# Optimization experiments

Measured on AMD Instinct MI355X. Metric: run time of the kernel, lower is better.

The kernel has to match this reference:

```python
import jax, jax.numpy as jnp
import numpy as np

N_ATOMS = 100000
M_NBR = 12
ORIG_FEA = 92
NBR_FEA = 41
AF = 64          # atom_fea_len
N_CONV = 3
OUT_DIM = 128
N_CRYSTALS = 2000
ATOMS_PER = 50
EPS = 1e-5


def setup_inputs() -> dict:
    key = jax.random.key(0)
    ks = jax.random.split(key, 12)
    inp = {
        "atom_fea": jax.random.normal(ks[0], (N_ATOMS, ORIG_FEA), dtype=jnp.float32),
        "nbr_fea": jax.random.normal(ks[1], (N_ATOMS, M_NBR, NBR_FEA), dtype=jnp.float32),
        "nbr_fea_idx": jax.random.randint(ks[2], (N_ATOMS, M_NBR), 0, N_ATOMS, dtype=jnp.int32),
        "crystal_atom_idx": jnp.arange(N_CRYSTALS * ATOMS_PER, dtype=jnp.int32).reshape(N_CRYSTALS, ATOMS_PER),
    }
    # parameters
    inp["W_embed"] = jax.random.normal(ks[3], (ORIG_FEA, AF), dtype=jnp.float32) * 0.05
    inp["b_embed"] = jnp.zeros((AF,), dtype=jnp.float32)
    in_full = 2 * AF + NBR_FEA  # 169
    inp["W_full"] = jax.random.normal(ks[4], (N_CONV, in_full, 2 * AF), dtype=jnp.float32) * 0.05
    inp["b_full"] = jnp.zeros((N_CONV, 2 * AF), dtype=jnp.float32)
    inp["bn1_gamma"] = jnp.ones((N_CONV, 2 * AF), dtype=jnp.float32)
    inp["bn1_beta"] = jnp.zeros((N_CONV, 2 * AF), dtype=jnp.float32)
    inp["bn2_gamma"] = jnp.ones((N_CONV, AF), dtype=jnp.float32)
    inp["bn2_beta"] = jnp.zeros((N_CONV, AF), dtype=jnp.float32)
    inp["W_pool"] = jax.random.normal(ks[5], (AF, OUT_DIM), dtype=jnp.float32) * 0.05
    inp["b_pool"] = jnp.zeros((OUT_DIM,), dtype=jnp.float32)
    return inp


def _batchnorm(x, gamma, beta):
    # training-mode BatchNorm1d over leading dim, biased variance
    m = jnp.mean(x, axis=0)
    v = jnp.var(x, axis=0)
    return (x - m) * jax.lax.rsqrt(v + EPS) * gamma + beta


def _conv_layer(x, nbr_fea, nbr_fea_idx, Wf, bf, g1, be1, g2, be2):
    N, M = nbr_fea_idx.shape
    nbr_atom = x[nbr_fea_idx]                                  # [N, M, AF] gather
    self_fea = jnp.broadcast_to(x[:, None, :], (N, M, AF))     # [N, M, AF]
    total = jnp.concatenate([self_fea, nbr_atom, nbr_fea], axis=2)  # [N, M, 2AF+NBR]
    gated = jnp.einsum('nmi,io->nmo', total, Wf) + bf          # [N, M, 2AF]
    gated = _batchnorm(gated.reshape(N * M, 2 * AF), g1, be1).reshape(N, M, 2 * AF)
    nbr_filter = jax.nn.sigmoid(gated[..., :AF])
    nbr_core = jax.nn.softplus(gated[..., AF:])
    nbr_sumed = jnp.sum(nbr_filter * nbr_core, axis=1)         # [N, AF]
    nbr_sumed = _batchnorm(nbr_sumed, g2, be2)
    return jax.nn.softplus(x + nbr_sumed)


def reference(atom_fea, nbr_fea, nbr_fea_idx, crystal_atom_idx,
              W_embed, b_embed, W_full, b_full,
              bn1_gamma, bn1_beta, bn2_gamma, bn2_beta,
              W_pool, b_pool):
    x = atom_fea @ W_embed + b_embed                           # [N, AF]
    for i in range(N_CONV):
        x = _conv_layer(x, nbr_fea, nbr_fea_idx,
                        W_full[i], b_full[i],
                        bn1_gamma[i], bn1_beta[i],
                        bn2_gamma[i], bn2_beta[i])
    crystal_fea = jnp.mean(x[crystal_atom_idx], axis=1)        # [G, AF] per-graph mean pool
    return jax.nn.relu(crystal_fea @ W_pool + b_pool)          # [G, OUT_DIM]
```

## Files before the change

### kernel.cpp

```cpp
#include <hip/hip_runtime.h>
#include <hip/hip_fp16.h>
#include <math.h>

#define N_ATOMS 100000
#define M_NBR 12
#define ORIG_FEA 92
#define NBR_FEA 41
#define AF 64
#define OUT2 128
#define IN_FULL 169
#define N_CONV 3
#define OUT_DIM 128
#define N_CRYSTALS 2000
#define ATOMS_PER 50
#define EPS 1e-5f

#define ZCH 16
#define EDGES (ZCH * M_NBR)
#define NF_STRIDE 44
#define YB_ATOMS 80
#define YB_CHUNK 16

__device__ __forceinline__ float softplus_f(float x) {
    return fmaxf(x, 0.0f) + __logf(1.0f + __expf(-fabsf(x)));
}
__device__ __forceinline__ float sigmoid_f(float x) {
    return __builtin_amdgcn_rcpf(1.0f + __expf(-x));
}
__device__ __forceinline__ void fma4(float4& a, float s, const float4& b) {
    a.x = fmaf(s, b.x, a.x); a.y = fmaf(s, b.y, a.y);
    a.z = fmaf(s, b.z, a.z); a.w = fmaf(s, b.w, a.w);
}
__device__ __forceinline__ float4 zero4() { return make_float4(0.f, 0.f, 0.f, 0.f); }
#define ELEM(v, kk) ((kk) == 0 ? (v).x : (kk) == 1 ? (v).y : (kk) == 2 ? (v).z : (v).w)

union H4 { uint2 u; __half2 h[2]; };
__device__ __forceinline__ void store_h4(__half* p, float4 v) {
    H4 t;
    t.h[0] = __floats2half2_rn(v.x, v.y);
    t.h[1] = __floats2half2_rn(v.z, v.w);
    *(uint2*)p = t.u;
}
__device__ __forceinline__ float4 load_h4(const __half* p) {
    H4 t; t.u = *(const uint2*)p;
    float2 a = __half22float2(t.h[0]);
    float2 b = __half22float2(t.h[1]);
    return make_float4(a.x, a.y, b.x, b.y);
}

__global__ __launch_bounds__(256, 2) void k_embed(
    const float* __restrict__ af, const float* __restrict__ W,
    const float* __restrict__ b, float* __restrict__ x) {
  __shared__ __align__(16) float saf[64 * ORIG_FEA];
  int a0 = blockIdx.x * 64;
  int na = min(64, N_ATOMS - a0);
  int tid = threadIdx.x;
  int c = tid & 63, rgrp = tid >> 6;
  float w[ORIG_FEA];
#pragma unroll
  for (int k = 0; k < ORIG_FEA; ++k) w[k] = W[k * AF + c];
  int n4 = na * (ORIG_FEA / 4);
  const float4* g4 = (const float4*)(af + (size_t)a0 * ORIG_FEA);
  float4* s4 = (float4*)saf;
  for (int e = tid; e < n4; e += 256) s4[e] = g4[e];
  __syncthreads();
  float bc = b[c];
  for (int a = rgrp; a < na; a += 4) {
    float acc = bc;
    const float4* row = (const float4*)(saf + a * ORIG_FEA);
#pragma unroll
    for (int q = 0; q < ORIG_FEA / 4; ++q) {
      float4 v = row[q];
      acc = fmaf(v.x, w[4 * q], acc);
      acc = fmaf(v.y, w[4 * q + 1], acc);
      acc = fmaf(v.z, w[4 * q + 2], acc);
      acc = fmaf(v.w, w[4 * q + 3], acc);
    }
    x[(size_t)(a0 + a) * AF + c] = acc;
  }
}

__global__ __launch_bounds__(256, 2) void k_ysn(
    const float* __restrict__ x, const float* __restrict__ Wf,
    float* __restrict__ y_self, float* __restrict__ y_nbr) {
  __shared__ __align__(16) float sW2[64 * 256];
  __shared__ __align__(16) float sx[YB_CHUNK * AF];
  int tid = threadIdx.x;
  int cg = tid & 31, ag = tid >> 5;
  int c0 = cg * 4;
  {
    float4* s4 = (float4*)sW2;
    const float4* g4 = (const float4*)Wf;
    for (int e = tid; e < 64 * 64; e += 256) {
      int r = e >> 6, q = e & 63;
      s4[r * 64 + q] = (q < 32) ? g4[r * 32 + q] : g4[(64 + r) * 32 + (q - 32)];
    }
  }
  int ab = blockIdx.x * YB_ATOMS;
  for (int cc = 0; cc < YB_ATOMS / YB_CHUNK; ++cc) {
    int a0 = ab + cc * YB_CHUNK;
    __syncthreads();
    {
      float4* s4 = (float4*)sx;
      const float4* g4 = (const float4*)(x + (size_t)a0 * AF);
      for (int e = tid; e < YB_CHUNK * AF / 4; e += 256) s4[e] = g4[e];
    }
    __syncthreads();
    float4 accs[2] = {zero4(), zero4()};
    float4 accn[2] = {zero4(), zero4()};
    for (int k0 = 0; k0 < AF; k0 += 4) {
      float4 av0 = *(const float4*)(sx + (ag * 2 + 0) * AF + k0);
      float4 av1 = *(const float4*)(sx + (ag * 2 + 1) * AF + k0);
#pragma unroll
      for (int kk = 0; kk < 4; ++kk) {
        float4 b0 = *(const float4*)(sW2 + (k0 + kk) * 256 + c0);
        float4 b1 = *(const float4*)(sW2 + (k0 + kk) * 256 + 128 + c0);
        float s0 = ELEM(av0, kk), s1 = ELEM(av1, kk);
        fma4(accs[0], s0, b0); fma4(accn[0], s0, b1);
        fma4(accs[1], s1, b0); fma4(accn[1], s1, b1);
      }
    }
#pragma unroll
    for (int t = 0; t < 2; ++t) {
      size_t n = (size_t)(a0 + ag * 2 + t);
      *(float4*)(y_self + n * OUT2 + c0) = accs[t];
      *(float4*)(y_nbr + n * OUT2 + c0) = accn[t];
    }
  }
}

__device__ __forceinline__ void edge_gemm(
    const float* snf, const float* sW, int ebase, int c0,
    float4 acc0[6], float4 acc1[6]) {
#pragma unroll
  for (int e = 0; e < 6; ++e) { acc0[e] = zero4(); acc1[e] = zero4(); }
  for (int k0 = 0; k0 < 40; k0 += 4) {
    float4 av[6];
#pragma unroll
    for (int e = 0; e < 6; ++e)
      av[e] = *(const float4*)(snf + (ebase + e) * NF_STRIDE + k0);
#pragma unroll
    for (int kk = 0; kk < 4; ++kk) {
      float4 b0 = *(const float4*)(sW + (k0 + kk) * OUT2 + c0);
      float4 b1 = *(const float4*)(sW + (k0 + kk) * OUT2 + AF + c0);
#pragma unroll
      for (int e = 0; e < 6; ++e) {
        float s = ELEM(av[e], kk);
        fma4(acc0[e], s, b0);
        fma4(acc1[e], s, b1);
      }
    }
  }
  {
    float4 b0 = *(const float4*)(sW + 40 * OUT2 + c0);
    float4 b1 = *(const float4*)(sW + 40 * OUT2 + AF + c0);
#pragma unroll
    for (int e = 0; e < 6; ++e) {
      float s = snf[(ebase + e) * NF_STRIDE + 40];
      fma4(acc0[e], s, b0);
      fma4(acc1[e], s, b1);
    }
  }
}

__device__ __forceinline__ void stage_edge(
    const float* __restrict__ nbr_fea, const int* __restrict__ nidx,
    const float* __restrict__ We, int a0, int tid,
    float* snf, float* sW, int* sidx) {
  float4* sW4 = (float4*)sW;
  const float4* gW4 = (const float4*)We;
  for (int e = tid; e < NBR_FEA * (OUT2 / 4); e += 256) sW4[e] = gW4[e];
  const float* gnf = nbr_fea + (size_t)a0 * M_NBR * NBR_FEA;
  for (int e = tid; e < EDGES * NBR_FEA; e += 256) {
    int r = e / NBR_FEA;
    int k = e - r * NBR_FEA;
    snf[r * NF_STRIDE + k] = gnf[e];
  }
  for (int e = tid; e < EDGES; e += 256) sidx[e] = nidx[(size_t)a0 * M_NBR + e];
}

template <int WZ>
__global__ __launch_bounds__(256, 2) void k_zstats_t(
    const float* __restrict__ nbr_fea, const int* __restrict__ nidx,
    const float* __restrict__ y_self, const float* __restrict__ y_nbr,
    const float* __restrict__ Wf, const float* __restrict__ bf,
    float* __restrict__ gsum, float* __restrict__ gsumsq,
    __half* __restrict__ z16) {
  __shared__ __align__(16) float snf[EDGES * NF_STRIDE];
  __shared__ __align__(16) float sW[NBR_FEA * OUT2];
  __shared__ int sidx[EDGES];
  __shared__ float lsum[OUT2], lsumsq[OUT2];
  int tid = threadIdx.x;
  int cg = tid & 15, eg = tid >> 4;
  int c0 = cg * 4;
  if (tid < OUT2) { lsum[tid] = 0.f; lsumsq[tid] = 0.f; }
  int a0 = blockIdx.x * ZCH;
  stage_edge(nbr_fea, nidx, Wf + 2 * AF * OUT2, a0, tid, snf, sW, sidx);
  __syncthreads();
  float4 bz0 = *(const float4*)(bf + c0);
  float4 bz1 = *(const float4*)(bf + AF + c0);
  float4 sm0 = zero4(), sq0 = zero4(), sm1 = zero4(), sq1 = zero4();
  for (int c = 0; c < 2; ++c) {
    int ebase = c * 96 + eg * 6;
    int atomL = c * 8 + (eg >> 1);
    const float* ys = y_self + (size_t)(a0 + atomL) * OUT2;
    float4 y0 = *(const float4*)(ys + c0);
    float4 y1 = *(const float4*)(ys + AF + c0);
    float4 acc0[6], acc1[6];
    edge_gemm(snf, sW, ebase, c0, acc0, acc1);
#pragma unroll
    for (int e = 0; e < 6; ++e) {
      int j = sidx[ebase + e];
      const float* yn = y_nbr + (size_t)j * OUT2;
      float4 n0 = *(const float4*)(yn + c0);
      float4 n1 = *(const float4*)(yn + AF + c0);
      float4 z0, z1;
      z0.x = acc0[e].x + y0.x + n0.x + bz0.x; z0.y = acc0[e].y + y0.y + n0.y + bz0.y;
      z0.z = acc0[e].z + y0.z + n0.z + bz0.z; z0.w = acc0[e].w + y0.w + n0.w + bz0.w;
      z1.x = acc1[e].x + y1.x + n1.x + bz1.x; z1.y = acc1[e].y + y1.y + n1.y + bz1.y;
      z1.z = acc1[e].z + y1.z + n1.z + bz1.z; z1.w = acc1[e].w + y1.w + n1.w + bz1.w;
      if (WZ) {
        __half* zp = z16 + ((size_t)a0 * M_NBR + ebase + e) * OUT2 + c0;
        store_h4(zp, z0);
        store_h4(zp + AF, z1);
      }
      sm0.x += z0.x; sm0.y += z0.y; sm0.z += z0.z; sm0.w += z0.w;
      sm1.x += z1.x; sm1.y += z1.y; sm1.z += z1.z; sm1.w += z1.w;
      sq0.x = fmaf(z0.x, z0.x, sq0.x); sq0.y = fmaf(z0.y, z0.y, sq0.y);
      sq0.z = fmaf(z0.z, z0.z, sq0.z); sq0.w = fmaf(z0.w, z0.w, sq0.w);
      sq1.x = fmaf(z1.x, z1.x, sq1.x); sq1.y = fmaf(z1.y, z1.y, sq1.y);
      sq1.z = fmaf(z1.z, z1.z, sq1.z); sq1.w = fmaf(z1.w, z1.w, sq1.w);
    }
  }
  atomicAdd(&lsum[c0 + 0], sm0.x); atomicAdd(&lsum[c0 + 1], sm0.y);
  atomicAdd(&lsum[c0 + 2], sm0.z); atomicAdd(&lsum[c0 + 3], sm0.w);
  atomicAdd(&lsum[AF + c0 + 0], sm1.x); atomicAdd(&lsum[AF + c0 + 1], sm1.y);
  atomicAdd(&lsum[AF + c0 + 2], sm1.z); atomicAdd(&lsum[AF + c0 + 3], sm1.w);
  atomicAdd(&lsumsq[c0 + 0], sq0.x); atomicAdd(&lsumsq[c0 + 1], sq0.y);
  atomicAdd(&lsumsq[c0 + 2], sq0.z); atomicAdd(&lsumsq[c0 + 3], sq0.w);
  atomicAdd(&lsumsq[AF + c0 + 0], sq1.x); atomicAdd(&lsumsq[AF + c0 + 1], sq1.y);
  atomicAdd(&lsumsq[AF + c0 + 2], sq1.z); atomicAdd(&lsumsq[AF + c0 + 3], sq1.w);
  __syncthreads();
  if (tid < OUT2) {
    atomicAdd(&gsum[tid], lsum[tid]);
    atomicAdd(&gsumsq[tid], lsumsq[tid]);
  }
}

__global__ __launch_bounds__(256, 4) void k_apply_stream(
    const __half* __restrict__ z16,
    const float* __restrict__ sc1, const float* __restrict__ sh1,
    float* __restrict__ s_out, float* __restrict__ gsum, float* __restrict__ gsumsq) {
  __shared__ float lsum[AF], lsumsq[AF];
  int tid = threadIdx.x;
  if (tid < AF) { lsum[tid] = 0.f; lsumsq[tid] = 0.f; }
  __syncthreads();
  int cg = tid & 15, a = tid >> 4;
  int c0 = cg * 4;
  size_t atom = (size_t)blockIdx.x * 16 + a;
  float4 f0 = *(const float4*)(sc1 + c0);
  float4 g0 = *(const float4*)(sh1 + c0);
  float4 f1 = *(const float4*)(sc1 + AF + c0);
  float4 g1 = *(const float4*)(sh1 + AF + c0);
  const __half* zr = z16 + atom * (M_NBR * OUT2);
  float4 sacc = zero4();
#pragma unroll 4
  for (int m = 0; m < M_NBR; ++m) {
    float4 zf = load_h4(zr + m * OUT2 + c0);
    float4 zc = load_h4(zr + m * OUT2 + AF + c0);
    zf.x = fmaf(zf.x, f0.x, g0.x); zf.y = fmaf(zf.y, f0.y, g0.y);
    zf.z = fmaf(zf.z, f0.z, g0.z); zf.w = fmaf(zf.w, f0.w, g0.w);
    zc.x = fmaf(zc.x, f1.x, g1.x); zc.y = fmaf(zc.y, f1.y, g1.y);
    zc.z = fmaf(zc.z, f1.z, g1.z); zc.w = fmaf(zc.w, f1.w, g1.w);
    sacc.x = fmaf(sigmoid_f(zf.x), softplus_f(zc.x), sacc.x);
    sacc.y = fmaf(sigmoid_f(zf.y), softplus_f(zc.y), sacc.y);
    sacc.z = fmaf(sigmoid_f(zf.z), softplus_f(zc.z), sacc.z);
    sacc.w = fmaf(sigmoid_f(zf.w), softplus_f(zc.w), sacc.w);
  }
  *(float4*)(s_out + atom * AF + c0) = sacc;
  float4 sq;
  sq.x = sacc.x * sacc.x; sq.y = sacc.y * sacc.y;
  sq.z = sacc.z * sacc.z; sq.w = sacc.w * sacc.w;
  sacc.x += __shfl_xor(sacc.x, 16, 64); sacc.y += __shfl_xor(sacc.y, 16, 64);
  sacc.z += __shfl_xor(sacc.z, 16, 64); sacc.w += __shfl_xor(sacc.w, 16, 64);
  sq.x += __shfl_xor(sq.x, 16, 64); sq.y += __shfl_xor(sq.y, 16, 64);
  sq.z += __shfl_xor(sq.z, 16, 64); sq.w += __shfl_xor(sq.w, 16, 64);
  sacc.x += __shfl_xor(sacc.x, 32, 64); sacc.y += __shfl_xor(sacc.y, 32, 64);
  sacc.z += __shfl_xor(sacc.z, 32, 64); sacc.w += __shfl_xor(sacc.w, 32, 64);
  sq.x += __shfl_xor(sq.x, 32, 64); sq.y += __shfl_xor(sq.y, 32, 64);
  sq.z += __shfl_xor(sq.z, 32, 64); sq.w += __shfl_xor(sq.w, 32, 64);
  if ((tid & 48) == 0) {
    atomicAdd(&lsum[c0 + 0], sacc.x); atomicAdd(&lsum[c0 + 1], sacc.y);
    atomicAdd(&lsum[c0 + 2], sacc.z); atomicAdd(&lsum[c0 + 3], sacc.w);
    atomicAdd(&lsumsq[c0 + 0], sq.x); atomicAdd(&lsumsq[c0 + 1], sq.y);
    atomicAdd(&lsumsq[c0 + 2], sq.z); atomicAdd(&lsumsq[c0 + 3], sq.w);
  }
  __syncthreads();
  if (tid < AF) {
    atomicAdd(&gsum[tid], lsum[tid]);
    atomicAdd(&gsumsq[tid], lsumsq[tid]);
  }
}

__global__ __launch_bounds__(256, 2) void k_apply(
    const float* __restrict__ nbr_fea, const int* __restrict__ nidx,
    const float* __restrict__ y_self, const float* __restrict__ y_nbr,
    const float* __restrict__ Wf, const float* __restrict__ bf,
    const float* __restrict__ sc1, const float* __restrict__ sh1,
    float* __restrict__ s_out, float* __restrict__ gsum, float* __restrict__ gsumsq) {
  __shared__ __align__(16) float snf[EDGES * NF_STRIDE];
  __shared__ __align__(16) float sW[NBR_FEA * OUT2];
  __shared__ int sidx[EDGES];
  __shared__ float lsum[AF], lsumsq[AF];
  int tid = threadIdx.x;
  int cg = tid & 15, eg = tid >> 4;
  int c0 = cg * 4;
  if (tid < AF) { lsum[tid] = 0.f; lsumsq[tid] = 0.f; }
  int a0 = blockIdx.x * ZCH;
  stage_edge(nbr_fea, nidx, Wf + 2 * AF * OUT2, a0, tid, snf, sW, sidx);
  __syncthreads();
  float4 bz0 = *(const float4*)(bf + c0);
  float4 bz1 = *(const float4*)(bf + AF + c0);
  float4 f0 = *(const float4*)(sc1 + c0);
  float4 g0 = *(const float4*)(sh1 + c0);
  float4 f1 = *(const float4*)(sc1 + AF + c0);
  float4 g1 = *(const float4*)(sh1 + AF + c0);
  float4 sm2 = zero4(), sq2 = zero4();
  for (int c = 0; c < 2; ++c) {
    int ebase = c * 96 + eg * 6;
    int atomL = c * 8 + (eg >> 1);
    const float* ys = y_self + (size_t)(a0 + atomL) * OUT2;
    float4 y0 = *(const float4*)(ys + c0);
    float4 y1 = *(const float4*)(ys + AF + c0);
    float4 acc0[6], acc1[6];
    edge_gemm(snf, sW, ebase, c0, acc0, acc1);
    float4 sacc = zero4();
#pragma unroll
    for (int e = 0; e < 6; ++e) {
      int j = sidx[ebase + e];
      const float* yn = y_nbr + (size_t)j * OUT2;
      float4 n0 = *(const float4*)(yn + c0);
      float4 n1 = *(const float4*)(yn + AF + c0);
      float4 z0, z1;
      z0.x = fmaf(acc0[e].x + y0.x + n0.x + bz0.x, f0.x, g0.x);
      z0.y = fmaf(acc0[e].y + y0.y + n0.y + bz0.y, f0.y, g0.y);
      z0.z = fmaf(acc0[e].z + y0.z + n0.z + bz0.z, f0.z, g0.z);
      z0.w = fmaf(acc0[e].w + y0.w + n0.w + bz0.w, f0.w, g0.w);
      z1.x = fmaf(acc1[e].x + y1.x + n1.x + bz1.x, f1.x, g1.x);
      z1.y = fmaf(acc1[e].y + y1.y + n1.y + bz1.y, f1.y, g1.y);
      z1.z = fmaf(acc1[e].z + y1.z + n1.z + bz1.z, f1.z, g1.z);
      z1.w = fmaf(acc1[e].w + y1.w + n1.w + bz1.w, f1.w, g1.w);
      sacc.x = fmaf(sigmoid_f(z0.x), softplus_f(z1.x), sacc.x);
      sacc.y = fmaf(sigmoid_f(z0.y), softplus_f(z1.y), sacc.y);
      sacc.z = fmaf(sigmoid_f(z0.z), softplus_f(z1.z), sacc.z);
      sacc.w = fmaf(sigmoid_f(z0.w), softplus_f(z1.w), sacc.w);
    }
    sacc.x += __shfl_xor(sacc.x, 16, 64);
    sacc.y += __shfl_xor(sacc.y, 16, 64);
    sacc.z += __shfl_xor(sacc.z, 16, 64);
    sacc.w += __shfl_xor(sacc.w, 16, 64);
    if ((eg & 1) == 0) {
      *(float4*)(s_out + (size_t)(a0 + atomL) * AF + c0) = sacc;
      sm2.x += sacc.x; sm2.y += sacc.y; sm2.z += sacc.z; sm2.w += sacc.w;
      sq2.x = fmaf(sacc.x, sacc.x, sq2.x); sq2.y = fmaf(sacc.y, sacc.y, sq2.y);
      sq2.z = fmaf(sacc.z, sacc.z, sq2.z); sq2.w = fmaf(sacc.w, sacc.w, sq2.w);
    }
  }
  if ((eg & 1) == 0) {
    atomicAdd(&lsum[c0 + 0], sm2.x); atomicAdd(&lsum[c0 + 1], sm2.y);
    atomicAdd(&lsum[c0 + 2], sm2.z); atomicAdd(&lsum[c0 + 3], sm2.w);
    atomicAdd(&lsumsq[c0 + 0], sq2.x); atomicAdd(&lsumsq[c0 + 1], sq2.y);
    atomicAdd(&lsumsq[c0 + 2], sq2.z); atomicAdd(&lsumsq[c0 + 3], sq2.w);
  }
  __syncthreads();
  if (tid < AF) {
    atomicAdd(&gsum[tid], lsum[tid]);
    atomicAdd(&gsumsq[tid], lsumsq[tid]);
  }
}

__global__ void k_finalize(const float* __restrict__ gsum, const float* __restrict__ gsumsq,
                           const float* __restrict__ gamma, const float* __restrict__ beta,
                           float* __restrict__ scale, float* __restrict__ shift,
                           int chn, float invcount) {
  int c = threadIdx.x;
  if (c < chn) {
    float m = gsum[c] * invcount;
    float v = gsumsq[c] * invcount - m * m;
    float sc = gamma[c] * rsqrtf(v + EPS);
    scale[c] = sc;
    shift[c] = beta[c] - m * sc;
  }
}

__global__ __launch_bounds__(256) void k_update(
    float* __restrict__ x, const float* __restrict__ s,
    const float* __restrict__ sc2, const float* __restrict__ sh2) {
  int e = blockIdx.x * 256 + threadIdx.x;
  if (e < N_ATOMS * AF) {
    int c = e & (AF - 1);
    float v = x[e] + s[e] * sc2[c] + sh2[c];
    x[e] = softplus_f(v);
  }
}

__global__ __launch_bounds__(128) void k_pool(
    const float* __restrict__ x, const int* __restrict__ cidx,
    const float* __restrict__ Wp, const float* __restrict__ bp,
    float* __restrict__ out) {
  __shared__ float part[2][AF];
  __shared__ float mean[AF];
  int g = blockIdx.x, tid = threadIdx.x;
  int c = tid & 63, h = tid >> 6;
  float acc = 0.f;
  for (int a = h; a < ATOMS_PER; a += 2) {
    int idx = cidx[g * ATOMS_PER + a];
    acc += x[(size_t)idx * AF + c];
  }
  part[h][c] = acc;
  __syncthreads();
  if (tid < AF) mean[tid] = (part[0][tid] + part[1][tid]) * (1.0f / ATOMS_PER);
  __syncthreads();
  float o = bp[tid];
#pragma unroll
  for (int k = 0; k < AF; ++k) o += mean[k] * Wp[k * OUT_DIM + tid];
  out[(size_t)g * OUT_DIM + tid] = fmaxf(o, 0.f);
}

extern "C" void kernel_launch(void* const* d_in, const int* in_sizes, int n_in,
                              void* d_out, int out_size, void* d_ws, size_t ws_size,
                              hipStream_t stream) {
  const float* atom_fea = (const float*)d_in[0];
  const float* nbr_fea  = (const float*)d_in[1];
  const int*   nbr_idx  = (const int*)d_in[2];
  const int*   cidx     = (const int*)d_in[3];
  const float* W_embed  = (const float*)d_in[4];
  const float* b_embed  = (const float*)d_in[5];
  const float* W_full   = (const float*)d_in[6];
  const float* b_full   = (const float*)d_in[7];
  const float* bn1_g    = (const float*)d_in[8];
  const float* bn1_b    = (const float*)d_in[9];
  const float* bn2_g    = (const float*)d_in[10];
  const float* bn2_b    = (const float*)d_in[11];
  const float* W_pool   = (const float*)d_in[12];
  const float* b_pool   = (const float*)d_in[13];
  float* out = (float*)d_out;

  float* ws = (float*)d_ws;
  size_t off = 0;
  float* x      = ws + off; off += (size_t)N_ATOMS * AF;
  float* y_self = ws + off; off += (size_t)N_ATOMS * OUT2;
  float* y_nbr  = ws + off; off += (size_t)N_ATOMS * OUT2;
  float* s_buf  = ws + off; off += (size_t)N_ATOMS * AF;
  float* sums   = ws + off; off += (size_t)N_CONV * 384;
  float* affine = ws + off; off += (size_t)N_CONV * 384;
  off = (off + 3) & ~(size_t)3;

  size_t z_bytes = (size_t)N_ATOMS * M_NBR * OUT2 * sizeof(__half);
  bool fast = ws_size >= off * sizeof(float) + z_bytes;
  __half* z16 = fast ? (__half*)(ws + off) : nullptr;

  hipMemsetAsync(sums, 0, (size_t)N_CONV * 384 * sizeof(float), stream);

  k_embed<<<(N_ATOMS + 63) / 64, 256, 0, stream>>>(atom_fea, W_embed, b_embed, x);

  for (int i = 0; i < N_CONV; ++i) {
    const float* Wf = W_full + (size_t)i * IN_FULL * OUT2;
    const float* bf = b_full + (size_t)i * OUT2;
    float* sum1   = sums + (size_t)i * 384;
    float* sumsq1 = sum1 + OUT2;
    float* sum2   = sumsq1 + OUT2;
    float* sumsq2 = sum2 + AF;
    float* sc1 = affine + (size_t)i * 384;
    float* sh1 = sc1 + OUT2;
    float* sc2 = sh1 + OUT2;
    float* sh2 = sc2 + AF;

    k_ysn<<<N_ATOMS / YB_ATOMS, 256, 0, stream>>>(x, Wf, y_self, y_nbr);
    if (fast) {
      k_zstats_t<1><<<N_ATOMS / ZCH, 256, 0, stream>>>(nbr_fea, nbr_idx, y_self, y_nbr,
                                                       Wf, bf, sum1, sumsq1, z16);
      k_finalize<<<1, 128, 0, stream>>>(sum1, sumsq1, bn1_g + i * OUT2, bn1_b + i * OUT2,
                                        sc1, sh1, OUT2, 1.0f / ((float)N_ATOMS * M_NBR));
      k_apply_stream<<<N_ATOMS / 16, 256, 0, stream>>>(z16, sc1, sh1, s_buf,
                                                       sum2, sumsq2);
    } else {
      k_zstats_t<0><<<N_ATOMS / ZCH, 256, 0, stream>>>(nbr_fea, nbr_idx, y_self, y_nbr,
                                                       Wf, bf, sum1, sumsq1, nullptr);
      k_finalize<<<1, 128, 0, stream>>>(sum1, sumsq1, bn1_g + i * OUT2, bn1_b + i * OUT2,
                                        sc1, sh1, OUT2, 1.0f / ((float)N_ATOMS * M_NBR));
      k_apply<<<N_ATOMS / ZCH, 256, 0, stream>>>(nbr_fea, nbr_idx, y_self, y_nbr,
                                                 Wf, bf, sc1, sh1, s_buf, sum2, sumsq2);
    }
    k_finalize<<<1, 128, 0, stream>>>(sum2, sumsq2, bn2_g + i * AF, bn2_b + i * AF,
                                      sc2, sh2, AF, 1.0f / (float)N_ATOMS);
    k_update<<<(N_ATOMS * AF + 255) / 256, 256, 0, stream>>>(x, s_buf, sc2, sh2);
  }

  k_pool<<<N_CRYSTALS, 128, 0, stream>>>(x, cidx, W_pool, b_pool, out);
}
```

Before: 2.190 ms.

## Use fp16 neighbor features with fdot2 edge GEMM and higher occupancy

Converts nbr_fea once per call into a padded fp16 buffer and stages it, plus pair-packed fp16 edge weights, into shared memory. The edge GEMM then uses the packed fp16 dot2 instruction instead of fp32 FMAs. Halving the shared-memory footprint lets launch bounds ask for four blocks per SM. This cuts LDS usage, global traffic for neighbor features and ALU work in the zstats kernel, at the cost of fp16 rounding of inputs and weights and one extra conversion pass.

```diff
diff --git a/kernel.cpp b/kernel.cpp
--- a/kernel.cpp
+++ b/kernel.cpp
@@ -17,9 +17,14 @@
 
 #define ZCH 16
 #define EDGES (ZCH * M_NBR)
-#define NF_STRIDE 44
+#define NFH_STRIDE 44
+#define KPAIRS 22
 #define YB_ATOMS 80
 #define YB_CHUNK 16
+#define NF_ROWS (N_ATOMS * M_NBR)
+
+typedef _Float16 h2 __attribute__((ext_vector_type(2)));
+typedef _Float16 h4 __attribute__((ext_vector_type(4)));
 
 __device__ __forceinline__ float softplus_f(float x) {
     return fmaxf(x, 0.0f) + __logf(1.0f + __expf(-fabsf(x)));
@@ -33,6 +38,16 @@
 }
 __device__ __forceinline__ float4 zero4() { return make_float4(0.f, 0.f, 0.f, 0.f); }
 #define ELEM(v, kk) ((kk) == 0 ? (v).x : (kk) == 1 ? (v).y : (kk) == 2 ? (v).z : (v).w)
+
+__device__ __forceinline__ float fdot2_(h2 a, h2 b, float c) {
+#if __has_builtin(__builtin_amdgcn_fdot2)
+    return __builtin_amdgcn_fdot2(a, b, c, false);
+#else
+    return fmaf((float)a[1], (float)b[1], fmaf((float)a[0], (float)b[0], c));
+#endif
+}
+__device__ __forceinline__ h2 lo2(h4 v) { h2 r; r[0] = v[0]; r[1] = v[1]; return r; }
+__device__ __forceinline__ h2 hi2(h4 v) { h2 r; r[0] = v[2]; r[1] = v[3]; return r; }
 
 union H4 { uint2 u; __half2 h[2]; };
 __device__ __forceinline__ void store_h4(__half* p, float4 v) {
@@ -78,6 +93,25 @@
     }
     x[(size_t)(a0 + a) * AF + c] = acc;
   }
+}
+
+__global__ __launch_bounds__(256) void k_nf16(
+    const float* __restrict__ nf, _Float16* __restrict__ out) {
+  int g = blockIdx.x * 256 + threadIdx.x;
+  if (g >= NF_ROWS * 11) return;
+  int row = g / 11;
+  int q = g - row * 11;
+  int k = 4 * q;
+  const float* in = nf + (size_t)row * NBR_FEA;
+  h4 v;
+  if (q == 10) {
+    v[0] = (_Float16)in[40];
+    v[1] = (_Float16)0.f; v[2] = (_Float16)0.f; v[3] = (_Float16)0.f;
+  } else {
+    v[0] = (_Float16)in[k];     v[1] = (_Float16)in[k + 1];
+    v[2] = (_Float16)in[k + 2]; v[3] = (_Float16)in[k + 3];
+  }
+  *(h4*)(out + (size_t)row * NFH_STRIDE + k) = v;
 }
 
 __global__ __launch_bounds__(256, 2) void k_ysn(
@@ -129,65 +163,80 @@
   }
 }
 
-__device__ __forceinline__ void edge_gemm(
-    const float* snf, const float* sW, int ebase, int c0,
+__device__ __forceinline__ void edge_gemm2(
+    const _Float16* snf, const h2* sWp, int ebase, int c0,
     float4 acc0[6], float4 acc1[6]) {
 #pragma unroll
   for (int e = 0; e < 6; ++e) { acc0[e] = zero4(); acc1[e] = zero4(); }
-  for (int k0 = 0; k0 < 40; k0 += 4) {
-    float4 av[6];
+#pragma unroll
+  for (int q = 0; q < 11; ++q) {
+    h4 av[6];
 #pragma unroll
     for (int e = 0; e < 6; ++e)
-      av[e] = *(const float4*)(snf + (ebase + e) * NF_STRIDE + k0);
-#pragma unroll
-    for (int kk = 0; kk < 4; ++kk) {
-      float4 b0 = *(const float4*)(sW + (k0 + kk) * OUT2 + c0);
-      float4 b1 = *(const float4*)(sW + (k0 + kk) * OUT2 + AF + c0);
+      av[e] = *(const h4*)(snf + (ebase + e) * NFH_STRIDE + 4 * q);
+#pragma unroll
+    for (int r = 0; r < 2; ++r) {
+      const h2* wr = sWp + (2 * q + r) * OUT2;
+      h2 wf0 = wr[c0], wf1 = wr[c0 + 1], wf2 = wr[c0 + 2], wf3 = wr[c0 + 3];
+      h2 wc0 = wr[AF + c0], wc1 = wr[AF + c0 + 1];
+      h2 wc2 = wr[AF + c0 + 2], wc3 = wr[AF + c0 + 3];
 #pragma unroll
       for (int e = 0; e < 6; ++e) {
-        float s = ELEM(av[e], kk);
-        fma4(acc0[e], s, b0);
-        fma4(acc1[e], s, b1);
+        h2 a = (r == 0) ? lo2(av[e]) : hi2(av[e]);
+        acc0[e].x = fdot2_(a, wf0, acc0[e].x);
+        acc0[e].y = fdot2_(a, wf1, acc0[e].y);
+        acc0[e].z = fdot2_(a, wf2, acc0[e].z);
+        acc0[e].w = fdot2_(a, wf3, acc0[e].w);
+        acc1[e].x = fdot2_(a, wc0, acc1[e].x);
+        acc1[e].y = fdot2_(a, wc1, acc1[e].y);
+        acc1[e].z = fdot2_(a, wc2, acc1[e].z);
+        acc1[e].w = fdot2_(a, wc3, acc1[e].w);
       }
     }
   }
-  {
-    float4 b0 = *(const float4*)(sW + 40 * OUT2 + c0);
-    float4 b1 = *(const float4*)(sW + 40 * OUT2 + AF + c0);
-#pragma unroll
-    for (int e = 0; e < 6; ++e) {
-      float s = snf[(ebase + e) * NF_STRIDE + 40];
-      fma4(acc0[e], s, b0);
-      fma4(acc1[e], s, b1);
-    }
-  }
-}
-
-__device__ __forceinline__ void stage_edge(
-    const float* __restrict__ nbr_fea, const int* __restrict__ nidx,
-    const float* __restrict__ We, int a0, int tid,
-    float* snf, float* sW, int* sidx) {
-  float4* sW4 = (float4*)sW;
-  const float4* gW4 = (const float4*)We;
-  for (int e = tid; e < NBR_FEA * (OUT2 / 4); e += 256) sW4[e] = gW4[e];
-  const float* gnf = nbr_fea + (size_t)a0 * M_NBR * NBR_FEA;
-  for (int e = tid; e < EDGES * NBR_FEA; e += 256) {
-    int r = e / NBR_FEA;
-    int k = e - r * NBR_FEA;
-    snf[r * NF_STRIDE + k] = gnf[e];
+}
+
+template <int NF16>
+__device__ __forceinline__ void stage_edge2(
+    const float* __restrict__ nbr_fea, const _Float16* __restrict__ nf16,
+    const int* __restrict__ nidx, const float* __restrict__ We,
+    int a0, int tid, _Float16* snf, h2* sWp, int* sidx) {
+  for (int idx = tid; idx < KPAIRS * OUT2; idx += 256) {
+    int kp = idx >> 7, c = idx & 127, k0 = kp * 2;
+    h2 v;
+    v[0] = (_Float16)((k0 <= 40) ? We[k0 * OUT2 + c] : 0.f);
+    v[1] = (_Float16)((k0 + 1 <= 40) ? We[(k0 + 1) * OUT2 + c] : 0.f);
+    sWp[idx] = v;
+  }
+  if (NF16) {
+    const uint4* g = (const uint4*)(nf16 + (size_t)a0 * M_NBR * NFH_STRIDE);
+    uint4* s = (uint4*)snf;
+    for (int e = tid; e < EDGES * NFH_STRIDE / 8; e += 256) s[e] = g[e];
+  } else {
+    const float* gnf = nbr_fea + (size_t)a0 * M_NBR * NBR_FEA;
+    for (int e = tid; e < EDGES * NBR_FEA; e += 256) {
+      int r = e / NBR_FEA, k = e - r * NBR_FEA;
+      snf[r * NFH_STRIDE + k] = (_Float16)gnf[e];
+    }
+    for (int e = tid; e < EDGES; e += 256) {
+      snf[e * NFH_STRIDE + 41] = (_Float16)0.f;
+      snf[e * NFH_STRIDE + 42] = (_Float16)0.f;
+      snf[e * NFH_STRIDE + 43] = (_Float16)0.f;
+    }
   }
   for (int e = tid; e < EDGES; e += 256) sidx[e] = nidx[(size_t)a0 * M_NBR + e];
 }
 
-template <int WZ>
-__global__ __launch_bounds__(256, 2) void k_zstats_t(
-    const float* __restrict__ nbr_fea, const int* __restrict__ nidx,
+template <int WZ, int NF16>
+__global__ __launch_bounds__(256, 4) void k_zstats_t(
+    const float* __restrict__ nbr_fea, const _Float16* __restrict__ nf16,
+    const int* __restrict__ nidx,
     const float* __restrict__ y_self, const float* __restrict__ y_nbr,
     const float* __restrict__ Wf, const float* __restrict__ bf,
     float* __restrict__ gsum, float* __restrict__ gsumsq,
     __half* __restrict__ z16) {
-  __shared__ __align__(16) float snf[EDGES * NF_STRIDE];
-  __shared__ __align__(16) float sW[NBR_FEA * OUT2];
+  __shared__ __align__(16) _Float16 snf[EDGES * NFH_STRIDE];
+  __shared__ __align__(16) h2 sWp[KPAIRS * OUT2];
   __shared__ int sidx[EDGES];
   __shared__ float lsum[OUT2], lsumsq[OUT2];
   int tid = threadIdx.x;
@@ -195,7 +244,7 @@
   int c0 = cg * 4;
   if (tid < OUT2) { lsum[tid] = 0.f; lsumsq[tid] = 0.f; }
   int a0 = blockIdx.x * ZCH;
-  stage_edge(nbr_fea, nidx, Wf + 2 * AF * OUT2, a0, tid, snf, sW, sidx);
+  stage_edge2<NF16>(nbr_fea, nf16, nidx, Wf + 2 * AF * OUT2, a0, tid, snf, sWp, sidx);
   __syncthreads();
   float4 bz0 = *(const float4*)(bf + c0);
   float4 bz1 = *(const float4*)(bf + AF + c0);
@@ -207,7 +256,7 @@
     float4 y0 = *(const float4*)(ys + c0);
     float4 y1 = *(const float4*)(ys + AF + c0);
     float4 acc0[6], acc1[6];
-    edge_gemm(snf, sW, ebase, c0, acc0, acc1);
+    edge_gemm2(snf, sWp, ebase, c0, acc0, acc1);
 #pragma unroll
     for (int e = 0; e < 6; ++e) {
       int j = sidx[ebase + e];
@@ -302,14 +351,14 @@
   }
 }
 
-__global__ __launch_bounds__(256, 2) void k_apply(
+__global__ __launch_bounds__(256, 4) void k_apply(
     const float* __restrict__ nbr_fea, const int* __restrict__ nidx,
     const float* __restrict__ y_self, const float* __restrict__ y_nbr,
     const float* __restrict__ Wf, const float* __restrict__ bf,
     const float* __restrict__ sc1, const float* __restrict__ sh1,
     float* __restrict__ s_out, float* __restrict__ gsum, float* __restrict__ gsumsq) {
-  __shared__ __align__(16) float snf[EDGES * NF_STRIDE];
-  __shared__ __align__(16) float sW[NBR_FEA * OUT2];
+  __shared__ __align__(16) _Float16 snf[EDGES * NFH_STRIDE];
+  __shared__ __align__(16) h2 sWp[KPAIRS * OUT2];
   __shared__ int sidx[EDGES];
   __shared__ float lsum[AF], lsumsq[AF];
   int tid = threadIdx.x;
@@ -317,7 +366,7 @@
   int c0 = cg * 4;
   if (tid < AF) { lsum[tid] = 0.f; lsumsq[tid] = 0.f; }
   int a0 = blockIdx.x * ZCH;
-  stage_edge(nbr_fea, nidx, Wf + 2 * AF * OUT2, a0, tid, snf, sW, sidx);
+  stage_edge2<0>(nbr_fea, nullptr, nidx, Wf + 2 * AF * OUT2, a0, tid, snf, sWp, sidx);
   __syncthreads();
   float4 bz0 = *(const float4*)(bf + c0);
   float4 bz1 = *(const float4*)(bf + AF + c0);
@@ -325,7 +374,6 @@
   float4 g0 = *(const float4*)(sh1 + c0);
   float4 f1 = *(const float4*)(sc1 + AF + c0);
   float4 g1 = *(const float4*)(sh1 + AF + c0);
-  float4 sm2 = zero4(), sq2 = zero4();
   for (int c = 0; c < 2; ++c) {
     int ebase = c * 96 + eg * 6;
     int atomL = c * 8 + (eg >> 1);
@@ -333,7 +381,7 @@
     float4 y0 = *(const float4*)(ys + c0);
     float4 y1 = *(const float4*)(ys + AF + c0);
     float4 acc0[6], acc1[6];
-    edge_gemm(snf, sW, ebase, c0, acc0, acc1);
+    edge_gemm2(snf, sWp, ebase, c0, acc0, acc1);
     float4 sacc = zero4();
 #pragma unroll
     for (int e = 0; e < 6; ++e) {
@@ -361,16 +409,13 @@
     sacc.w += __shfl_xor(sacc.w, 16, 64);
     if ((eg & 1) == 0) {
       *(float4*)(s_out + (size_t)(a0 + atomL) * AF + c0) = sacc;
-      sm2.x += sacc.x; sm2.y += sacc.y; sm2.z += sacc.z; sm2.w += sacc.w;
-      sq2.x = fmaf(sacc.x, sacc.x, sq2.x); sq2.y = fmaf(sacc.y, sacc.y, sq2.y);
-      sq2.z = fmaf(sacc.z, sacc.z, sq2.z); sq2.w = fmaf(sacc.w, sacc.w, sq2.w);
-    }
-  }
-  if ((eg & 1) == 0) {
-    atomicAdd(&lsum[c0 + 0], sm2.x); atomicAdd(&lsum[c0 + 1], sm2.y);
-    atomicAdd(&lsum[c0 + 2], sm2.z); atomicAdd(&lsum[c0 + 3], sm2.w);
-    atomicAdd(&lsumsq[c0 + 0], sq2.x); atomicAdd(&lsumsq[c0 + 1], sq2.y);
-    atomicAdd(&lsumsq[c0 + 2], sq2.z); atomicAdd(&lsumsq[c0 + 3], sq2.w);
+      atomicAdd(&lsum[c0 + 0], sacc.x); atomicAdd(&lsum[c0 + 1], sacc.y);
+      atomicAdd(&lsum[c0 + 2], sacc.z); atomicAdd(&lsum[c0 + 3], sacc.w);
+      atomicAdd(&lsumsq[c0 + 0], sacc.x * sacc.x);
+      atomicAdd(&lsumsq[c0 + 1], sacc.y * sacc.y);
+      atomicAdd(&lsumsq[c0 + 2], sacc.z * sacc.z);
+      atomicAdd(&lsumsq[c0 + 3], sacc.w * sacc.w);
+    }
   }
   __syncthreads();
   if (tid < AF) {
@@ -456,11 +501,18 @@
   float* affine = ws + off; off += (size_t)N_CONV * 384;
   off = (off + 3) & ~(size_t)3;
 
-  size_t z_bytes = (size_t)N_ATOMS * M_NBR * OUT2 * sizeof(__half);
-  bool fast = ws_size >= off * sizeof(float) + z_bytes;
-  __half* z16 = fast ? (__half*)(ws + off) : nullptr;
+  size_t base_bytes = off * sizeof(float);
+  size_t z_bytes  = (size_t)N_ATOMS * M_NBR * OUT2 * sizeof(__half);
+  size_t nf_bytes = (size_t)N_ATOMS * M_NBR * NFH_STRIDE * sizeof(_Float16);
+  bool fast  = ws_size >= base_bytes + z_bytes;
+  bool fast2 = ws_size >= base_bytes + z_bytes + nf_bytes;
+  __half* z16 = fast ? (__half*)((char*)d_ws + base_bytes) : nullptr;
+  _Float16* nf16 = fast2 ? (_Float16*)((char*)d_ws + base_bytes + z_bytes) : nullptr;
 
   hipMemsetAsync(sums, 0, (size_t)N_CONV * 384 * sizeof(float), stream);
+
+  if (fast2)
+    k_nf16<<<(NF_ROWS * 11 + 255) / 256, 256, 0, stream>>>(nbr_fea, nf16);
 
   k_embed<<<(N_ATOMS + 63) / 64, 256, 0, stream>>>(atom_fea, W_embed, b_embed, x);
 
@@ -477,18 +529,22 @@
     float* sh2 = sc2 + AF;
 
     k_ysn<<<N_ATOMS / YB_ATOMS, 256, 0, stream>>>(x, Wf, y_self, y_nbr);
+    if (fast2) {
+      k_zstats_t<1, 1><<<N_ATOMS / ZCH, 256, 0, stream>>>(
+          nbr_fea, nf16, nbr_idx, y_self, y_nbr, Wf, bf, sum1, sumsq1, z16);
+    } else if (fast) {
+      k_zstats_t<1, 0><<<N_ATOMS / ZCH, 256, 0, stream>>>(
+          nbr_fea, nullptr, nbr_idx, y_self, y_nbr, Wf, bf, sum1, sumsq1, z16);
+    } else {
+      k_zstats_t<0, 0><<<N_ATOMS / ZCH, 256, 0, stream>>>(
+          nbr_fea, nullptr, nbr_idx, y_self, y_nbr, Wf, bf, sum1, sumsq1, nullptr);
+    }
+    k_finalize<<<1, 128, 0, stream>>>(sum1, sumsq1, bn1_g + i * OUT2, bn1_b + i * OUT2,
+                                      sc1, sh1, OUT2, 1.0f / ((float)N_ATOMS * M_NBR));
     if (fast) {
-      k_zstats_t<1><<<N_ATOMS / ZCH, 256, 0, stream>>>(nbr_fea, nbr_idx, y_self, y_nbr,
-                                                       Wf, bf, sum1, sumsq1, z16);
-      k_finalize<<<1, 128, 0, stream>>>(sum1, sumsq1, bn1_g + i * OUT2, bn1_b + i * OUT2,
-                                        sc1, sh1, OUT2, 1.0f / ((float)N_ATOMS * M_NBR));
       k_apply_stream<<<N_ATOMS / 16, 256, 0, stream>>>(z16, sc1, sh1, s_buf,
                                                        sum2, sumsq2);
     } else {
-      k_zstats_t<0><<<N_ATOMS / ZCH, 256, 0, stream>>>(nbr_fea, nbr_idx, y_self, y_nbr,
-                                                       Wf, bf, sum1, sumsq1, nullptr);
-      k_finalize<<<1, 128, 0, stream>>>(sum1, sumsq1, bn1_g + i * OUT2, bn1_b + i * OUT2,
-                                        sc1, sh1, OUT2, 1.0f / ((float)N_ATOMS * M_NBR));
       k_apply<<<N_ATOMS / ZCH, 256, 0, stream>>>(nbr_fea, nbr_idx, y_self, y_nbr,
                                                  Wf, bf, sc1, sh1, s_buf, sum2, sumsq2);
     }
```

After: 3.964 ms. 81.0% more time.
